# Optimization experiments

Hardware: AMD Instinct MI355X
Metric: run time of the kernel (lower is better)

Reference implementation:

```python
import jax, jax.numpy as jnp
import numpy as np

B, T, D = 2, 2048, 2048
N, KH, H = 16, 8, 128  # query heads, kv heads, head_dim
S = 2048               # cache size
EPS = 1e-6
ROPE_THETA = 1000000.0
K_MASK = -0.7 * float(np.finfo(np.float32).max)  # jax _get_large_negative(float32)


def _rms_norm(x, w):
    rms = jnp.sqrt(jnp.mean(x.astype(jnp.float32) ** 2, axis=-1, keepdims=True) + EPS)
    return (w * x / rms).astype(x.dtype)


def _rope_embeddings(positions, head_dim):
    fraction = jnp.arange(0, head_dim, 2, dtype=jnp.float32) / head_dim
    inv_freq = 1.0 / (ROPE_THETA ** fraction)
    sinusoid = jnp.einsum('BT,k->BTk', positions.astype(jnp.float32), inv_freq,
                          precision=jax.lax.Precision.HIGHEST)
    return jnp.sin(sinusoid), jnp.cos(sinusoid)


def _apply_rope(x, sin, cos):
    h = x.shape[-1] // 2
    x1, x2 = x[..., :h], x[..., h:]
    s, c = sin[:, :, None, :], cos[:, :, None, :]
    return jnp.concatenate([x1 * c - x2 * s, x2 * c + x1 * s], axis=-1).astype(x.dtype)


def _positions_from_segment_ids(seg):
    t = seg.shape[1]
    pos = jnp.arange(t, dtype=jnp.int32)[None, :] - jnp.argmax(seg, axis=1)[:, None]
    return jnp.where(seg != 0, pos, 2 ** 30)


def _num_left_pad(seg):
    return jnp.sum(jnp.cumsum(seg != 0, axis=-1) == 0, axis=-1).astype(jnp.int32)


def _attention(x, q_w, k_w, v_w, o_w, q_norm_w, k_norm_w, k_cache, v_cache,
               segment_ids, start_ind, cur_ind):
    b, t, _ = x.shape
    s = k_cache.shape[1]
    n, kh, h = q_w.shape[1], k_w.shape[1], q_w.shape[2]

    q = _rms_norm(jnp.einsum('BTD,DNH->BTNH', x, q_w), q_norm_w)  # [B,T,N,H]
    k = _rms_norm(jnp.einsum('BSD,DKH->BSKH', x, k_w), k_norm_w)  # [B,T,K,H]
    v = jnp.einsum('BSD,DKH->BSKH', x, v_w)                       # [B,T,K,H]

    start = jnp.where(start_ind < 0, _num_left_pad(segment_ids), start_ind)
    pos = _positions_from_segment_ids(segment_ids) + cur_ind
    sin, cos = _rope_embeddings(pos, h)
    q = _apply_rope(q, sin, cos)
    k = _apply_rope(k, sin, cos)

    # KV-cache update at cur_ind
    k_cache = jax.lax.dynamic_update_slice(k_cache, k, (0, cur_ind, 0, 0))
    v_cache = jax.lax.dynamic_update_slice(v_cache, v, (0, cur_ind, 0, 0))

    # GQA: group query heads per kv head
    qg = q.reshape(b, t, kh, n // kh, h)
    logits = jnp.einsum('BTHGD,BSHD->BHGTS', qg, k_cache) * (h ** -0.5)

    q_pos = cur_ind + jnp.arange(t, dtype=jnp.int32)[None, :] - start[:, None]  # [B,T]
    ts = jnp.arange(s, dtype=jnp.int32)
    kv_seg = (ts[None, :] >= start[:, None]) & (ts[None, :] < cur_ind + t)      # [B,S] bool
    k_pos = ts[None, :] - start[:, None]                                        # [B,S]
    causal = k_pos[:, None, :] <= q_pos[:, :, None]                             # [B,T,S]
    # faithful to original: bool kv segment ids compared against int segment_ids
    seg_mask = kv_seg[:, None, :].astype(segment_ids.dtype) == segment_ids[:, :, None]
    final_mask = (causal & seg_mask)[:, None, None, :, :]                       # [B,1,1,T,S]

    logits = jnp.where(final_mask, logits, K_MASK)
    attn = jax.nn.softmax(logits.astype(jnp.float32), axis=-1).astype(logits.dtype)
    o = jnp.einsum('BHGTS,BSHD->BTHGD', attn, v_cache).reshape(b, t, n, h)
    return jnp.einsum('BTNH,NHD->BTD', o, o_w)


def setup_inputs() -> dict:
    key = jax.random.key(0)
    ks = jax.random.split(key, 5)
    scale = 0.02
    return {
        'x': jax.random.normal(ks[0], (B, T, D), jnp.float32),
        'q_w': jax.random.normal(ks[1], (D, N, H), jnp.float32) * scale,
        'k_w': jax.random.normal(ks[2], (D, KH, H), jnp.float32) * scale,
        'v_w': jax.random.normal(ks[3], (D, KH, H), jnp.float32) * scale,
        'o_w': jax.random.normal(ks[4], (N, H, D), jnp.float32) * scale,
        'q_norm_w': jnp.ones((H,), jnp.float32),
        'k_norm_w': jnp.ones((H,), jnp.float32),
        'k_cache': jnp.zeros((B, S, KH, H), jnp.float32),
        'v_cache': jnp.zeros((B, S, KH, H), jnp.float32),
        'segment_ids': jnp.ones((B, T), jnp.int32),
        'start_ind': jnp.zeros((B,), jnp.int32),
        'cur_ind': 0,
        'right_pads': 0,
    }


def reference(x, q_w, k_w, v_w, o_w, q_norm_w, k_norm_w, k_cache, v_cache,
              segment_ids, start_ind, cur_ind, right_pads):
    # right_pads only advances the cache write pointer (stateful side effect); it
    # does not affect the attention output.
    return _attention(x, q_w, k_w, v_w, o_w, q_norm_w, k_norm_w,
                      k_cache, v_cache, segment_ids, start_ind, cur_ind)
```

## Files before the change

kernel.cpp:

```cpp
#include <hip/hip_runtime.h>
#include <hip/hip_fp16.h>
#include <climits>
#include <math.h>

#define Bc   2
#define Tc   2048
#define Dc   2048
#define Nc   16
#define KHc  8
#define Hc   128
#define Sc   2048

constexpr float EPSc   = 1e-6f;
constexpr float SCALE2 = 0.1275174477984469f;

typedef short short8 __attribute__((ext_vector_type(8)));
typedef _Float16 half8 __attribute__((ext_vector_type(8)));
typedef __fp16 fp16x2 __attribute__((ext_vector_type(2)));
typedef float float4v __attribute__((ext_vector_type(4)));

union U16x8 { uint4 u; short8 s8; half8 h8; unsigned short us[8]; };
union H2U  { fp16x2 h; unsigned u; };
union S8H8 { short8 s; half8 h; };

__device__ __forceinline__ unsigned short f2bf(float f) {
    union { float f; unsigned u; } v; v.f = f;
    unsigned r = v.u + 0x7FFFu + ((v.u >> 16) & 1u);
    return (unsigned short)(r >> 16);
}
__device__ __forceinline__ float bf2f(unsigned short u) {
    union { unsigned u; float f; } v; v.u = ((unsigned)u) << 16;
    return v.f;
}

__device__ __forceinline__ void tc_body(const float* __restrict__ in,
                                        unsigned short* __restrict__ out,
                                        int R, int C, int bx, int by, int tid,
                                        float tile[32][33])
{
    int c0 = bx * 32, r0 = by * 32;
#pragma unroll
    for (int i = 0; i < 4; ++i) {
        int row = (tid >> 5) + i * 8, col = tid & 31;
        tile[row][col] = in[(size_t)(r0 + row) * C + c0 + col];
    }
    __syncthreads();
#pragma unroll
    for (int i = 0; i < 4; ++i) {
        int rowo = (tid >> 5) + i * 8, colo = tid & 31;
        out[(size_t)(c0 + rowo) * R + r0 + colo] = f2bf(tile[colo][rowo]);
    }
}

__global__ __launch_bounds__(256) void prep(const float* __restrict__ x,
                                            const float* __restrict__ qw,
                                            const float* __restrict__ kw,
                                            const float* __restrict__ vw,
                                            const float* __restrict__ ow,
                                            const int* __restrict__ seg,
                                            const int* __restrict__ start_ind,
                                            int* __restrict__ meta,
                                            unsigned short* __restrict__ xb,
                                            unsigned short* __restrict__ qkvwT,
                                            unsigned short* __restrict__ owT)
{
    __shared__ float tile[32][33];
    __shared__ int s_max, s_amax, s_nz;
    int id = blockIdx.x;
    int tid = threadIdx.x;

    if (id < Bc) {
        int b = id;
        if (tid == 0) { s_max = INT_MIN; s_amax = Tc; s_nz = Tc; }
        __syncthreads();
        int lmax = INT_MIN;
        for (int t = tid; t < Tc; t += 256) lmax = max(lmax, seg[b * Tc + t]);
        atomicMax(&s_max, lmax);
        __syncthreads();
        int mv = s_max;
        int lamax = Tc, lnz = Tc;
        for (int t = tid; t < Tc; t += 256) {
            int v = seg[b * Tc + t];
            if (v == mv) lamax = min(lamax, t);
            if (v != 0)  lnz   = min(lnz, t);
        }
        atomicMin(&s_amax, lamax);
        atomicMin(&s_nz, lnz);
        __syncthreads();
        if (tid == 0) {
            meta[b] = s_amax;
            int st = start_ind[b];
            meta[Bc + b] = (st < 0) ? s_nz : st;
        }
        return;
    }
    id -= Bc;
    if (id < 4096) {
        size_t base = ((size_t)id * 256 + tid) * 8;
        float4 a = *(const float4*)&x[base];
        float4 b = *(const float4*)&x[base + 4];
        U16x8 o;
        o.us[0] = f2bf(a.x); o.us[1] = f2bf(a.y); o.us[2] = f2bf(a.z); o.us[3] = f2bf(a.w);
        o.us[4] = f2bf(b.x); o.us[5] = f2bf(b.y); o.us[6] = f2bf(b.z); o.us[7] = f2bf(b.w);
        *(uint4*)&xb[base] = o.u;
        return;
    }
    id -= 4096;
    if (id < 4096) { tc_body(qw, qkvwT, 2048, 2048, id & 63, id >> 6, tid, tile); return; }
    id -= 4096;
    if (id < 2048) { tc_body(kw, qkvwT + (size_t)2048 * 2048, 2048, 1024, id & 31, id >> 5, tid, tile); return; }
    id -= 2048;
    if (id < 2048) { tc_body(vw, qkvwT + (size_t)3072 * 2048, 2048, 1024, id & 31, id >> 5, tid, tile); return; }
    id -= 2048;
    tc_body(ow, owT, 2048, 2048, id & 63, id >> 6, tid, tile);
}

__global__ __launch_bounds__(256, 2) void gemm_mfma(const unsigned short* __restrict__ A,
                                                    const unsigned short* __restrict__ BT,
                                                    void* __restrict__ Cout,
                                                    int M, int N, int K, int out_fp32)
{
    __shared__ __align__(16) unsigned short As[128 * 32];
    __shared__ __align__(16) unsigned short Bs[128 * 32];
    int tid = threadIdx.x;
    int lane = tid & 63, w = tid >> 6;
    int quad = lane >> 4, l15 = lane & 15;
    int bm = blockIdx.y * 128, bn = blockIdx.x * 128;
    int wm = (w >> 1) * 64, wn = (w & 1) * 64;

    int srow = lane >> 2;
    int pl   = lane & 3;
    int sw   = (quad ^ ((l15 >> 1) & 3)) * 8;

    float4v acc[16];
#pragma unroll
    for (int i = 0; i < 16; ++i) acc[i] = (float4v)0.f;

    for (int k0 = 0; k0 < K; k0 += 32) {
        __syncthreads();
#pragma unroll
        for (int c = 0; c < 2; ++c) {
            int j = w * 2 + c;
            int row = j * 16 + srow;
            int pg = pl ^ ((row >> 1) & 3);
            __builtin_amdgcn_global_load_lds(
                (__attribute__((address_space(1))) void*)(A + (size_t)(bm + row) * K + k0 + pg * 8),
                (__attribute__((address_space(3))) void*)(As + j * 512), 16, 0, 0);
            __builtin_amdgcn_global_load_lds(
                (__attribute__((address_space(1))) void*)(BT + (size_t)(bn + row) * K + k0 + pg * 8),
                (__attribute__((address_space(3))) void*)(Bs + j * 512), 16, 0, 0);
        }
        __syncthreads();
        short8 af[4];
#pragma unroll
        for (int mi = 0; mi < 4; ++mi)
            af[mi] = *(const short8*)&As[(wm + mi * 16 + l15) * 32 + sw];
#pragma unroll
        for (int ni = 0; ni < 4; ++ni) {
            short8 bf = *(const short8*)&Bs[(wn + ni * 16 + l15) * 32 + sw];
#pragma unroll
            for (int mi = 0; mi < 4; ++mi)
                acc[mi * 4 + ni] = __builtin_amdgcn_mfma_f32_16x16x32_bf16(af[mi], bf, acc[mi * 4 + ni], 0, 0, 0);
        }
    }

#pragma unroll
    for (int mi = 0; mi < 4; ++mi)
#pragma unroll
        for (int ni = 0; ni < 4; ++ni)
#pragma unroll
            for (int reg = 0; reg < 4; ++reg) {
                int row = bm + wm + mi * 16 + quad * 4 + reg;
                int col = bn + wn + ni * 16 + l15;
                float v = acc[mi * 4 + ni][reg];
                if (out_fp32) ((float*)Cout)[(size_t)row * N + col] = v;
                else ((unsigned short*)Cout)[(size_t)row * N + col] = f2bf(v);
            }
}

__global__ __launch_bounds__(256) void post(unsigned short* __restrict__ QKVh,
                                            unsigned short* __restrict__ Kall,
                                            unsigned short* __restrict__ Vt,
                                            const float* __restrict__ qw,
                                            const float* __restrict__ kw,
                                            const int* __restrict__ seg,
                                            const int* __restrict__ meta,
                                            const int* __restrict__ cur_ptr,
                                            const float* __restrict__ kc,
                                            const float* __restrict__ vc)
{
    int id = blockIdx.x;
    int tid = threadIdx.x;
    int cur = cur_ptr[0];

    if (id < 24576) {
        int rowid = id * 4 + (tid >> 6);
        int lane = tid & 63;
        int hh = rowid % 24;
        int bt = rowid / 24;
        int t = bt & (Tc - 1);
        int b = bt >> 11;

        const unsigned short* in;
        unsigned short* out;
        const float* wt;
        if (hh < 16) {
            unsigned short* p = QKVh + (size_t)bt * 4096 + hh * Hc;
            in = p; out = p; wt = qw;
        } else {
            int kh = hh - 16;
            in = QKVh + (size_t)bt * 4096 + 2048 + kh * Hc;
            out = Kall + (((size_t)b * Sc + cur + t) * KHc + kh) * Hc;
            wt = kw;
        }
        float v1 = bf2f(in[lane]), v2 = bf2f(in[lane + 64]);
        float ssq = v1 * v1 + v2 * v2;
#pragma unroll
        for (int off = 1; off < 64; off <<= 1) ssq += __shfl_xor(ssq, off);
        float rinv = rsqrtf(ssq * (1.0f / Hc) + EPSc);

        int sg = seg[bt];
        long long pos = (sg != 0) ? (long long)(t - meta[b]) : (long long)(1 << 30);
        float posf = (float)(pos + (long long)cur);
        float inv_freq = exp2f(-(float)lane * (19.931568569324174f / 64.0f));
        float s, c;
        sincosf(posf * inv_freq, &s, &c);

        float n1 = wt[lane] * v1 * rinv;
        float n2 = wt[lane + 64] * v2 * rinv;
        out[lane]      = f2bf(n1 * c - n2 * s);
        out[lane + 64] = f2bf(n2 * c + n1 * s);
        return;
    }
    id -= 24576;
    if (id < 2048) {
        size_t base = ((size_t)id * 256 + tid) * 8;
        int s = (int)((base >> 10) & (Sc - 1));
        if (s >= cur && s < cur + Tc) return;
        float4 a = *(const float4*)&kc[base];
        float4 b = *(const float4*)&kc[base + 4];
        U16x8 o;
        o.us[0] = f2bf(a.x); o.us[1] = f2bf(a.y); o.us[2] = f2bf(a.z); o.us[3] = f2bf(a.w);
        o.us[4] = f2bf(b.x); o.us[5] = f2bf(b.y); o.us[6] = f2bf(b.z); o.us[7] = f2bf(b.w);
        *(uint4*)&Kall[base] = o.u;
        return;
    }
    id -= 2048;
    {
        int gid = id * 256 + tid;
        int h  = gid & 127;
        int s8 = ((gid >> 7) & 255) * 8;
        int kh = (gid >> 15) & 7;
        int b  = gid >> 18;
        int curT = cur + Tc;
        unsigned short tmp[8];
#pragma unroll
        for (int e = 0; e < 8; ++e) {
            int s = s8 + e;
            float f;
            if (s >= cur && s < curT)
                f = bf2f(QKVh[(size_t)(b * Tc + (s - cur)) * 4096 + 3072 + kh * Hc + h]);
            else
                f = vc[((size_t)(b * Sc + s) * KHc + kh) * Hc + h];
            tmp[e] = __half_as_ushort(__float2half(f));
        }
        *(uint4*)&Vt[(((size_t)b * KHc + kh) * Hc + h) * Sc + s8] = *(uint4*)tmp;
    }
}

__global__ __launch_bounds__(256, 2) void flash_mfma(const unsigned short* __restrict__ Qb,
                                                     const unsigned short* __restrict__ Kall,
                                                     const unsigned short* __restrict__ Vt,
                                                     const int* __restrict__ seg,
                                                     const int* __restrict__ meta,
                                                     const int* __restrict__ cur_ptr,
                                                     unsigned short* __restrict__ Ob)
{
    __shared__ __align__(16) unsigned short Ks[64 * 128];
    __shared__ __align__(16) unsigned short Vs[128 * 64];
    __shared__ __align__(16) unsigned short Ps[128 * 72];

    int tid = threadIdx.x;
    int lane = tid & 63, w = tid >> 6;
    int quad = lane >> 4, l15 = lane & 15;
    int bid = blockIdx.x;
    int raw = bid & 15;
    int n  = (bid >> 4) & 15;
    int b  = bid >> 8;
    int qt = (b == 0) ? raw : (15 - raw);
    int kh = n >> 1;
    int cur = cur_ptr[0];
    int startb = meta[Bc + b];
    int curT = cur + Tc;
    int t0 = qt * 128 + w * 32;

    short8 qf[2][4];
#pragma unroll
    for (int qtile = 0; qtile < 2; ++qtile)
#pragma unroll
        for (int ks = 0; ks < 4; ++ks) {
            int row = t0 + qtile * 16 + l15;
            U16x8 u;
            u.u = *(const uint4*)&Qb[(size_t)(b * Tc + row) * 4096 + n * Hc + ks * 32 + quad * 8];
            qf[qtile][ks] = u.s8;
        }

    int ctq[2], clsq[2];
#pragma unroll
    for (int qtile = 0; qtile < 2; ++qtile) {
        int trow = t0 + qtile * 16 + l15;
        int sg = seg[b * Tc + trow];
        clsq[qtile] = (sg == 0) ? 0 : ((sg == 1) ? 1 : 2);
        ctq[qtile] = cur + trow;
    }
    unsigned long long m0 = __ballot(clsq[0] == 1);
    unsigned long long m1 = __ballot(clsq[1] == 1);
    bool allseg1 = ((m0 & m1) == 0xFFFFFFFFFFFFFFFFull);

    float lsum[2] = {0.f, 0.f};
    float4v oT[16];
#pragma unroll
    for (int i = 0; i < 16; ++i) oT[i] = (float4v)0.f;

    int s_end = min(Sc, cur + qt * 128 + 128);
    int nch = (s_end + 63) >> 6;

    const size_t kstride = (size_t)KHc * Hc;
    const unsigned short* kptr[4];
    unsigned short* kdst[4];
#pragma unroll
    for (int i = 0; i < 4; ++i) {
        int j = w * 4 + i;
        int row = j * 4 + (lane >> 4);
        int pl = lane & 15;
        int pg = pl ^ ((row >> 1) & 7);
        kptr[i] = Kall + (size_t)b * Sc * kstride + (size_t)row * kstride + kh * Hc + pg * 8;
        kdst[i] = Ks + j * 512;
    }
    const unsigned short* vptr[4];
    unsigned short* vdst[4];
#pragma unroll
    for (int i = 0; i < 4; ++i) {
        int j = w * 4 + i;
        int h = j * 8 + (lane >> 3);
        int pl = lane & 7;
        int pg = pl ^ ((h >> 1) & 7);
        vptr[i] = Vt + ((size_t)b * KHc + kh) * (size_t)Hc * Sc + (size_t)h * Sc + pg * 8;
        vdst[i] = Vs + j * 512;
    }
    int sw3 = (l15 >> 1) & 7;
    unsigned short* psrow0 = Ps + (w * 32 + l15) * 72;
    unsigned short* psrow1 = Ps + (w * 32 + 16 + l15) * 72;

    for (int c = 0; c < nch; ++c) {
        int s0 = c * 64;
#pragma unroll
        for (int i = 0; i < 4; ++i) {
            __builtin_amdgcn_global_load_lds(
                (__attribute__((address_space(1))) void*)(kptr[i] + (size_t)s0 * kstride),
                (__attribute__((address_space(3))) void*)kdst[i], 16, 0, 0);
            __builtin_amdgcn_global_load_lds(
                (__attribute__((address_space(1))) void*)(vptr[i] + s0),
                (__attribute__((address_space(3))) void*)vdst[i], 16, 0, 0);
        }
        __syncthreads();

        float4v st[4][2];
#pragma unroll
        for (int i = 0; i < 4; ++i) { st[i][0] = (float4v)0.f; st[i][1] = (float4v)0.f; }
#pragma unroll
        for (int ks = 0; ks < 4; ++ks) {
#pragma unroll
            for (int stile = 0; stile < 4; ++stile) {
                short8 kf = *(const short8*)&Ks[(stile * 16 + l15) * 128 + ((ks * 4 + quad) ^ sw3) * 8];
                st[stile][0] = __builtin_amdgcn_mfma_f32_16x16x32_bf16(kf, qf[0][ks], st[stile][0], 0, 0, 0);
                st[stile][1] = __builtin_amdgcn_mfma_f32_16x16x32_bf16(kf, qf[1][ks], st[stile][1], 0, 0, 0);
            }
        }

        bool fullok = allseg1 && (s0 >= startb) && (s0 + 63 <= cur + t0) && (s0 + 63 < curT);

#pragma unroll
        for (int stile = 0; stile < 4; ++stile) {
#pragma unroll
            for (int qtile = 0; qtile < 2; ++qtile) {
                float p0, p1, p2, p3;
                if (fullok) {
                    p0 = exp2f(st[stile][qtile][0] * SCALE2);
                    p1 = exp2f(st[stile][qtile][1] * SCALE2);
                    p2 = exp2f(st[stile][qtile][2] * SCALE2);
                    p3 = exp2f(st[stile][qtile][3] * SCALE2);
                } else {
                    int ctv = ctq[qtile], clsv = clsq[qtile];
                    float pp[4];
#pragma unroll
                    for (int reg = 0; reg < 4; ++reg) {
                        int s = s0 + stile * 16 + quad * 4 + reg;
                        int kvseg = (s >= startb && s < curT) ? 1 : 0;
                        bool ok = (s <= ctv) && (clsv == kvseg);
                        pp[reg] = exp2f(ok ? st[stile][qtile][reg] * SCALE2 : -1e30f);
                    }
                    p0 = pp[0]; p1 = pp[1]; p2 = pp[2]; p3 = pp[3];
                }
                lsum[qtile] += (p0 + p1) + (p2 + p3);
                H2U a, d;
                a.h = __builtin_amdgcn_cvt_pkrtz(p0, p1);
                d.h = __builtin_amdgcn_cvt_pkrtz(p2, p3);
                uint2 pk; pk.x = a.u; pk.y = d.u;
                unsigned short* pr = (qtile == 0) ? psrow0 : psrow1;
                *(uint2*)&pr[stile * 16 + quad * 4] = pk;
            }
        }

#pragma unroll
        for (int kk = 0; kk < 2; ++kk) {
            S8H8 pf0, pf1;
            pf0.s = *(const short8*)&psrow0[kk * 32 + quad * 8];
            pf1.s = *(const short8*)&psrow1[kk * 32 + quad * 8];
#pragma unroll
            for (int htile = 0; htile < 8; ++htile) {
                S8H8 vf;
                vf.s = *(const short8*)&Vs[(htile * 16 + l15) * 64 + ((kk * 4 + quad) ^ sw3) * 8];
                oT[htile * 2 + 0] = __builtin_amdgcn_mfma_f32_16x16x32_f16(vf.h, pf0.h, oT[htile * 2 + 0], 0, 0, 0);
                oT[htile * 2 + 1] = __builtin_amdgcn_mfma_f32_16x16x32_f16(vf.h, pf1.h, oT[htile * 2 + 1], 0, 0, 0);
            }
        }
        __syncthreads();
    }

    float linv[2];
#pragma unroll
    for (int qtile = 0; qtile < 2; ++qtile) {
        float l = lsum[qtile];
        l += __shfl_xor(l, 16);
        l += __shfl_xor(l, 32);
        linv[qtile] = (l > 0.f) ? (1.0f / l) : 0.f;
    }

#pragma unroll
    for (int qtile = 0; qtile < 2; ++qtile) {
        int trow = t0 + qtile * 16 + l15;
        size_t base = ((size_t)(b * Tc + trow) * Nc + n) * Hc;
#pragma unroll
        for (int htile = 0; htile < 8; ++htile) {
            float4v v = oT[htile * 2 + qtile];
            unsigned short r0 = f2bf(v[0] * linv[qtile]);
            unsigned short r1 = f2bf(v[1] * linv[qtile]);
            unsigned short r2 = f2bf(v[2] * linv[qtile]);
            unsigned short r3 = f2bf(v[3] * linv[qtile]);
            uint2 pk;
            pk.x = (unsigned)r0 | ((unsigned)r1 << 16);
            pk.y = (unsigned)r2 | ((unsigned)r3 << 16);
            *(uint2*)&Ob[base + htile * 16 + quad * 4] = pk;
        }
    }
}

extern "C" void kernel_launch(void* const* d_in, const int* in_sizes, int n_in,
                              void* d_out, int out_size, void* d_ws, size_t ws_size,
                              hipStream_t stream)
{
    const float* x        = (const float*)d_in[0];
    const float* q_w      = (const float*)d_in[1];
    const float* k_w      = (const float*)d_in[2];
    const float* v_w      = (const float*)d_in[3];
    const float* o_w      = (const float*)d_in[4];
    const float* q_norm_w = (const float*)d_in[5];
    const float* k_norm_w = (const float*)d_in[6];
    const float* k_cache  = (const float*)d_in[7];
    const float* v_cache  = (const float*)d_in[8];
    const int*   seg      = (const int*)d_in[9];
    const int*   startind = (const int*)d_in[10];
    const int*   cur_ptr  = (const int*)d_in[11];
    (void)in_sizes; (void)n_in; (void)out_size; (void)ws_size;

    char* base = (char*)d_ws;
    int* meta = (int*)base;
    unsigned short* QKVh = (unsigned short*)(base + 1024);
    unsigned short* Kall = (unsigned short*)(base + 33555456);
    unsigned short* Vt   = (unsigned short*)(base + 41944064);
    unsigned short* xb   = (unsigned short*)(base + 50332672);
    unsigned short* qkvwT= (unsigned short*)(base + 67109888);
    unsigned short* owT  = (unsigned short*)(base + 83887104);
    unsigned short* Ob   = xb;

    prep<<<Bc + 4096 + 4096 + 2048 + 2048 + 4096, 256, 0, stream>>>(
        x, q_w, k_w, v_w, o_w, seg, startind, meta, xb, qkvwT, owT);

    gemm_mfma<<<dim3(32, 32), 256, 0, stream>>>(xb, qkvwT, QKVh, Bc * Tc, 4096, Dc, 0);

    post<<<24576 + 2048 + 2048, 256, 0, stream>>>(QKVh, Kall, Vt,
        q_norm_w, k_norm_w, seg, meta, cur_ptr, k_cache, v_cache);

    flash_mfma<<<Bc * Nc * (Tc / 128), 256, 0, stream>>>(QKVh, Kall, Vt, seg, meta, cur_ptr, Ob);

    gemm_mfma<<<dim3(16, 32), 256, 0, stream>>>(Ob, owT, d_out, Bc * Tc, Dc, Nc * Hc, 1);
}
```

Baseline: 396.2 us.

## Double-buffer K/V tiles in flash kernel with async prefetch and swizzled P

```diff
diff --git a/kernel.cpp b/kernel.cpp
--- a/kernel.cpp
+++ b/kernel.cpp
@@ -276,9 +276,9 @@
                                                      const int* __restrict__ cur_ptr,
                                                      unsigned short* __restrict__ Ob)
 {
-    __shared__ __align__(16) unsigned short Ks[64 * 128];
-    __shared__ __align__(16) unsigned short Vs[128 * 64];
-    __shared__ __align__(16) unsigned short Ps[128 * 72];
+    __shared__ __align__(16) unsigned short Ks[2][64 * 128];
+    __shared__ __align__(16) unsigned short Vs[2][128 * 64];
+    __shared__ __align__(16) unsigned short Ps[128 * 64];
 
     int tid = threadIdx.x;
     int lane = tid & 63, w = tid >> 6;
@@ -327,7 +327,6 @@
 
     const size_t kstride = (size_t)KHc * Hc;
     const unsigned short* kptr[4];
-    unsigned short* kdst[4];
 #pragma unroll
     for (int i = 0; i < 4; ++i) {
         int j = w * 4 + i;
@@ -335,10 +334,8 @@
         int pl = lane & 15;
         int pg = pl ^ ((row >> 1) & 7);
         kptr[i] = Kall + (size_t)b * Sc * kstride + (size_t)row * kstride + kh * Hc + pg * 8;
-        kdst[i] = Ks + j * 512;
     }
     const unsigned short* vptr[4];
-    unsigned short* vdst[4];
 #pragma unroll
     for (int i = 0; i < 4; ++i) {
         int j = w * 4 + i;
@@ -346,37 +343,62 @@
         int pl = lane & 7;
         int pg = pl ^ ((h >> 1) & 7);
         vptr[i] = Vt + ((size_t)b * KHc + kh) * (size_t)Hc * Sc + (size_t)h * Sc + pg * 8;
-        vdst[i] = Vs + j * 512;
-    }
+    }
+    const int jbase = w * 4 * 512;
     int sw3 = (l15 >> 1) & 7;
-    unsigned short* psrow0 = Ps + (w * 32 + l15) * 72;
-    unsigned short* psrow1 = Ps + (w * 32 + 16 + l15) * 72;
+    int sw8 = l15 & 7;
+    unsigned short* psrow0 = Ps + (w * 32 + l15) * 64;
+    unsigned short* psrow1 = Ps + (w * 32 + 16 + l15) * 64;
+
+#pragma unroll
+    for (int i = 0; i < 4; ++i) {
+        __builtin_amdgcn_global_load_lds(
+            (__attribute__((address_space(1))) void*)(kptr[i]),
+            (__attribute__((address_space(3))) void*)(&Ks[0][jbase + i * 512]), 16, 0, 0);
+        __builtin_amdgcn_global_load_lds(
+            (__attribute__((address_space(1))) void*)(vptr[i]),
+            (__attribute__((address_space(3))) void*)(&Vs[0][jbase + i * 512]), 16, 0, 0);
+    }
 
     for (int c = 0; c < nch; ++c) {
+        const int pb = c & 1;
+        const unsigned short* ksb = &Ks[pb][0];
+        const unsigned short* vsb = &Vs[pb][0];
         int s0 = c * 64;
-#pragma unroll
-        for (int i = 0; i < 4; ++i) {
-            __builtin_amdgcn_global_load_lds(
-                (__attribute__((address_space(1))) void*)(kptr[i] + (size_t)s0 * kstride),
-                (__attribute__((address_space(3))) void*)kdst[i], 16, 0, 0);
-            __builtin_amdgcn_global_load_lds(
-                (__attribute__((address_space(1))) void*)(vptr[i] + s0),
-                (__attribute__((address_space(3))) void*)vdst[i], 16, 0, 0);
-        }
-        __syncthreads();
+
+        if (c + 1 < nch) {
+            const int nb = pb ^ 1;
+            const int s1 = s0 + 64;
+#pragma unroll
+            for (int i = 0; i < 4; ++i) {
+                __builtin_amdgcn_global_load_lds(
+                    (__attribute__((address_space(1))) void*)(kptr[i] + (size_t)s1 * kstride),
+                    (__attribute__((address_space(3))) void*)(&Ks[nb][jbase + i * 512]), 16, 0, 0);
+                __builtin_amdgcn_global_load_lds(
+                    (__attribute__((address_space(1))) void*)(vptr[i] + s1),
+                    (__attribute__((address_space(3))) void*)(&Vs[nb][jbase + i * 512]), 16, 0, 0);
+            }
+            asm volatile("s_waitcnt vmcnt(8)" ::: "memory");
+        } else {
+            asm volatile("s_waitcnt vmcnt(0)" ::: "memory");
+        }
+        __builtin_amdgcn_s_barrier();
+        asm volatile("" ::: "memory");
 
         float4v st[4][2];
 #pragma unroll
         for (int i = 0; i < 4; ++i) { st[i][0] = (float4v)0.f; st[i][1] = (float4v)0.f; }
+        __builtin_amdgcn_s_setprio(1);
 #pragma unroll
         for (int ks = 0; ks < 4; ++ks) {
 #pragma unroll
             for (int stile = 0; stile < 4; ++stile) {
-                short8 kf = *(const short8*)&Ks[(stile * 16 + l15) * 128 + ((ks * 4 + quad) ^ sw3) * 8];
+                short8 kf = *(const short8*)&ksb[(stile * 16 + l15) * 128 + ((ks * 4 + quad) ^ sw3) * 8];
                 st[stile][0] = __builtin_amdgcn_mfma_f32_16x16x32_bf16(kf, qf[0][ks], st[stile][0], 0, 0, 0);
                 st[stile][1] = __builtin_amdgcn_mfma_f32_16x16x32_bf16(kf, qf[1][ks], st[stile][1], 0, 0, 0);
             }
         }
+        __builtin_amdgcn_s_setprio(0);
 
         bool fullok = allseg1 && (s0 >= startb) && (s0 + 63 <= cur + t0) && (s0 + 63 < curT);
 
@@ -408,24 +430,28 @@
                 d.h = __builtin_amdgcn_cvt_pkrtz(p2, p3);
                 uint2 pk; pk.x = a.u; pk.y = d.u;
                 unsigned short* pr = (qtile == 0) ? psrow0 : psrow1;
-                *(uint2*)&pr[stile * 16 + quad * 4] = pk;
+                *(uint2*)&pr[(((stile * 2 + (quad >> 1)) ^ sw8) << 3) + (quad & 1) * 4] = pk;
             }
         }
 
+        __builtin_amdgcn_s_setprio(1);
 #pragma unroll
         for (int kk = 0; kk < 2; ++kk) {
             S8H8 pf0, pf1;
-            pf0.s = *(const short8*)&psrow0[kk * 32 + quad * 8];
-            pf1.s = *(const short8*)&psrow1[kk * 32 + quad * 8];
+            pf0.s = *(const short8*)&psrow0[((kk * 4 + quad) ^ sw8) << 3];
+            pf1.s = *(const short8*)&psrow1[((kk * 4 + quad) ^ sw8) << 3];
 #pragma unroll
             for (int htile = 0; htile < 8; ++htile) {
                 S8H8 vf;
-                vf.s = *(const short8*)&Vs[(htile * 16 + l15) * 64 + ((kk * 4 + quad) ^ sw3) * 8];
+                vf.s = *(const short8*)&vsb[(htile * 16 + l15) * 64 + ((kk * 4 + quad) ^ sw3) * 8];
                 oT[htile * 2 + 0] = __builtin_amdgcn_mfma_f32_16x16x32_f16(vf.h, pf0.h, oT[htile * 2 + 0], 0, 0, 0);
                 oT[htile * 2 + 1] = __builtin_amdgcn_mfma_f32_16x16x32_f16(vf.h, pf1.h, oT[htile * 2 + 1], 0, 0, 0);
             }
         }
-        __syncthreads();
+        __builtin_amdgcn_s_setprio(0);
+
+        asm volatile("" ::: "memory");
+        __builtin_amdgcn_s_barrier();
     }
 
     float linv[2];
```

New measurement: 397.2 us. About the same (+0.2%).

## Shrink flash attention blocks to 64 query rows with reordered grid and swizzled P

Applied to the files above, without the earlier changes.

```diff
diff --git a/kernel.cpp b/kernel.cpp
--- a/kernel.cpp
+++ b/kernel.cpp
@@ -268,31 +268,38 @@
     }
 }
 
-__global__ __launch_bounds__(256, 2) void flash_mfma(const unsigned short* __restrict__ Qb,
-                                                     const unsigned short* __restrict__ Kall,
-                                                     const unsigned short* __restrict__ Vt,
-                                                     const int* __restrict__ seg,
-                                                     const int* __restrict__ meta,
-                                                     const int* __restrict__ cur_ptr,
-                                                     unsigned short* __restrict__ Ob)
+__global__ __launch_bounds__(128) void flash_mfma(const unsigned short* __restrict__ Qb,
+                                                  const unsigned short* __restrict__ Kall,
+                                                  const unsigned short* __restrict__ Vt,
+                                                  const int* __restrict__ seg,
+                                                  const int* __restrict__ meta,
+                                                  const int* __restrict__ cur_ptr,
+                                                  unsigned short* __restrict__ Ob)
 {
     __shared__ __align__(16) unsigned short Ks[64 * 128];
     __shared__ __align__(16) unsigned short Vs[128 * 64];
-    __shared__ __align__(16) unsigned short Ps[128 * 72];
+    __shared__ __align__(16) unsigned short Ps[64 * 64];
 
     int tid = threadIdx.x;
     int lane = tid & 63, w = tid >> 6;
     int quad = lane >> 4, l15 = lane & 15;
     int bid = blockIdx.x;
-    int raw = bid & 15;
-    int n  = (bid >> 4) & 15;
-    int b  = bid >> 8;
-    int qt = (b == 0) ? raw : (15 - raw);
+
+    int k4 = bid >> 8;
+    int u  = (bid >> 5) & 7;
+    int bn = bid & 31;
+    int qt;
+    if      (k4 == 0) qt = u;
+    else if (k4 == 1) qt = 15 - u;
+    else if (k4 == 2) qt = 16 + u;
+    else              qt = 31 - u;
+    int b = bn >> 4;
+    int n = bn & 15;
     int kh = n >> 1;
     int cur = cur_ptr[0];
     int startb = meta[Bc + b];
     int curT = cur + Tc;
-    int t0 = qt * 128 + w * 32;
+    int t0 = qt * 64 + w * 32;
 
     short8 qf[2][4];
 #pragma unroll
@@ -300,9 +307,9 @@
 #pragma unroll
         for (int ks = 0; ks < 4; ++ks) {
             int row = t0 + qtile * 16 + l15;
-            U16x8 u;
-            u.u = *(const uint4*)&Qb[(size_t)(b * Tc + row) * 4096 + n * Hc + ks * 32 + quad * 8];
-            qf[qtile][ks] = u.s8;
+            U16x8 uq;
+            uq.u = *(const uint4*)&Qb[(size_t)(b * Tc + row) * 4096 + n * Hc + ks * 32 + quad * 8];
+            qf[qtile][ks] = uq.s8;
         }
 
     int ctq[2], clsq[2];
@@ -322,26 +329,26 @@
 #pragma unroll
     for (int i = 0; i < 16; ++i) oT[i] = (float4v)0.f;
 
-    int s_end = min(Sc, cur + qt * 128 + 128);
+    int s_end = min(Sc, cur + qt * 64 + 64);
     int nch = (s_end + 63) >> 6;
 
     const size_t kstride = (size_t)KHc * Hc;
-    const unsigned short* kptr[4];
-    unsigned short* kdst[4];
-#pragma unroll
-    for (int i = 0; i < 4; ++i) {
-        int j = w * 4 + i;
+    const unsigned short* kptr[8];
+    unsigned short* kdst[8];
+#pragma unroll
+    for (int i = 0; i < 8; ++i) {
+        int j = w * 8 + i;
         int row = j * 4 + (lane >> 4);
         int pl = lane & 15;
         int pg = pl ^ ((row >> 1) & 7);
         kptr[i] = Kall + (size_t)b * Sc * kstride + (size_t)row * kstride + kh * Hc + pg * 8;
         kdst[i] = Ks + j * 512;
     }
-    const unsigned short* vptr[4];
-    unsigned short* vdst[4];
-#pragma unroll
-    for (int i = 0; i < 4; ++i) {
-        int j = w * 4 + i;
+    const unsigned short* vptr[8];
+    unsigned short* vdst[8];
+#pragma unroll
+    for (int i = 0; i < 8; ++i) {
+        int j = w * 8 + i;
         int h = j * 8 + (lane >> 3);
         int pl = lane & 7;
         int pg = pl ^ ((h >> 1) & 7);
@@ -349,13 +356,14 @@
         vdst[i] = Vs + j * 512;
     }
     int sw3 = (l15 >> 1) & 7;
-    unsigned short* psrow0 = Ps + (w * 32 + l15) * 72;
-    unsigned short* psrow1 = Ps + (w * 32 + 16 + l15) * 72;
+    int sw8 = l15 & 7;
+    unsigned short* psrow0 = Ps + (w * 32 + l15) * 64;
+    unsigned short* psrow1 = Ps + (w * 32 + 16 + l15) * 64;
 
     for (int c = 0; c < nch; ++c) {
         int s0 = c * 64;
 #pragma unroll
-        for (int i = 0; i < 4; ++i) {
+        for (int i = 0; i < 8; ++i) {
             __builtin_amdgcn_global_load_lds(
                 (__attribute__((address_space(1))) void*)(kptr[i] + (size_t)s0 * kstride),
                 (__attribute__((address_space(3))) void*)kdst[i], 16, 0, 0);
@@ -368,6 +376,7 @@
         float4v st[4][2];
 #pragma unroll
         for (int i = 0; i < 4; ++i) { st[i][0] = (float4v)0.f; st[i][1] = (float4v)0.f; }
+        __builtin_amdgcn_s_setprio(1);
 #pragma unroll
         for (int ks = 0; ks < 4; ++ks) {
 #pragma unroll
@@ -377,6 +386,7 @@
                 st[stile][1] = __builtin_amdgcn_mfma_f32_16x16x32_bf16(kf, qf[1][ks], st[stile][1], 0, 0, 0);
             }
         }
+        __builtin_amdgcn_s_setprio(0);
 
         bool fullok = allseg1 && (s0 >= startb) && (s0 + 63 <= cur + t0) && (s0 + 63 < curT);
 
@@ -408,15 +418,16 @@
                 d.h = __builtin_amdgcn_cvt_pkrtz(p2, p3);
                 uint2 pk; pk.x = a.u; pk.y = d.u;
                 unsigned short* pr = (qtile == 0) ? psrow0 : psrow1;
-                *(uint2*)&pr[stile * 16 + quad * 4] = pk;
+                *(uint2*)&pr[(((stile * 2 + (quad >> 1)) ^ sw8) << 3) + (quad & 1) * 4] = pk;
             }
         }
 
+        __builtin_amdgcn_s_setprio(1);
 #pragma unroll
         for (int kk = 0; kk < 2; ++kk) {
             S8H8 pf0, pf1;
-            pf0.s = *(const short8*)&psrow0[kk * 32 + quad * 8];
-            pf1.s = *(const short8*)&psrow1[kk * 32 + quad * 8];
+            pf0.s = *(const short8*)&psrow0[((kk * 4 + quad) ^ sw8) << 3];
+            pf1.s = *(const short8*)&psrow1[((kk * 4 + quad) ^ sw8) << 3];
 #pragma unroll
             for (int htile = 0; htile < 8; ++htile) {
                 S8H8 vf;
@@ -425,6 +436,8 @@
                 oT[htile * 2 + 1] = __builtin_amdgcn_mfma_f32_16x16x32_f16(vf.h, pf1.h, oT[htile * 2 + 1], 0, 0, 0);
             }
         }
+        __builtin_amdgcn_s_setprio(0);
+
         __syncthreads();
     }
 
@@ -492,7 +505,7 @@
     post<<<24576 + 2048 + 2048, 256, 0, stream>>>(QKVh, Kall, Vt,
         q_norm_w, k_norm_w, seg, meta, cur_ptr, k_cache, v_cache);
 
-    flash_mfma<<<Bc * Nc * (Tc / 128), 256, 0, stream>>>(QKVh, Kall, Vt, seg, meta, cur_ptr, Ob);
+    flash_mfma<<<Bc * Nc * (Tc / 64), 128, 0, stream>>>(QKVh, Kall, Vt, seg, meta, cur_ptr, Ob);
 
     gemm_mfma<<<dim3(16, 32), 256, 0, stream>>>(Ob, owT, d_out, Bc * Tc, Dc, Nc * Hc, 1);
 }
```

Measured after the change: 416.7 us. +5.2%, slower.

## Split flash attention work across 8 waves with 16 query rows each

Applied to the files above, without the earlier changes.

```diff
diff --git a/kernel.cpp b/kernel.cpp
--- a/kernel.cpp
+++ b/kernel.cpp
@@ -268,7 +268,7 @@
     }
 }
 
-__global__ __launch_bounds__(256, 2) void flash_mfma(const unsigned short* __restrict__ Qb,
+__global__ __launch_bounds__(512, 4) void flash_mfma(const unsigned short* __restrict__ Qb,
                                                      const unsigned short* __restrict__ Kall,
                                                      const unsigned short* __restrict__ Vt,
                                                      const int* __restrict__ seg,
@@ -278,7 +278,7 @@
 {
     __shared__ __align__(16) unsigned short Ks[64 * 128];
     __shared__ __align__(16) unsigned short Vs[128 * 64];
-    __shared__ __align__(16) unsigned short Ps[128 * 72];
+    __shared__ __align__(16) unsigned short Ps[128 * 64];
 
     int tid = threadIdx.x;
     int lane = tid & 63, w = tid >> 6;
@@ -292,56 +292,49 @@
     int cur = cur_ptr[0];
     int startb = meta[Bc + b];
     int curT = cur + Tc;
-    int t0 = qt * 128 + w * 32;
-
-    short8 qf[2][4];
-#pragma unroll
-    for (int qtile = 0; qtile < 2; ++qtile)
-#pragma unroll
-        for (int ks = 0; ks < 4; ++ks) {
-            int row = t0 + qtile * 16 + l15;
-            U16x8 u;
-            u.u = *(const uint4*)&Qb[(size_t)(b * Tc + row) * 4096 + n * Hc + ks * 32 + quad * 8];
-            qf[qtile][ks] = u.s8;
-        }
-
-    int ctq[2], clsq[2];
-#pragma unroll
-    for (int qtile = 0; qtile < 2; ++qtile) {
-        int trow = t0 + qtile * 16 + l15;
-        int sg = seg[b * Tc + trow];
-        clsq[qtile] = (sg == 0) ? 0 : ((sg == 1) ? 1 : 2);
-        ctq[qtile] = cur + trow;
-    }
-    unsigned long long m0 = __ballot(clsq[0] == 1);
-    unsigned long long m1 = __ballot(clsq[1] == 1);
-    bool allseg1 = ((m0 & m1) == 0xFFFFFFFFFFFFFFFFull);
-
-    float lsum[2] = {0.f, 0.f};
-    float4v oT[16];
-#pragma unroll
-    for (int i = 0; i < 16; ++i) oT[i] = (float4v)0.f;
+    int t0 = qt * 128 + w * 16;
+
+    short8 qf[4];
+#pragma unroll
+    for (int ks = 0; ks < 4; ++ks) {
+        int row = t0 + l15;
+        U16x8 uq;
+        uq.u = *(const uint4*)&Qb[(size_t)(b * Tc + row) * 4096 + n * Hc + ks * 32 + quad * 8];
+        qf[ks] = uq.s8;
+    }
+
+    int trow0 = t0 + l15;
+    int sg0 = seg[b * Tc + trow0];
+    int cls = (sg0 == 0) ? 0 : ((sg0 == 1) ? 1 : 2);
+    int ct  = cur + trow0;
+    unsigned long long mball = __ballot(cls == 1);
+    bool allseg1 = (mball == 0xFFFFFFFFFFFFFFFFull);
+
+    float lsum = 0.f;
+    float4v oT[8];
+#pragma unroll
+    for (int i = 0; i < 8; ++i) oT[i] = (float4v)0.f;
 
     int s_end = min(Sc, cur + qt * 128 + 128);
     int nch = (s_end + 63) >> 6;
 
     const size_t kstride = (size_t)KHc * Hc;
-    const unsigned short* kptr[4];
-    unsigned short* kdst[4];
-#pragma unroll
-    for (int i = 0; i < 4; ++i) {
-        int j = w * 4 + i;
+    const unsigned short* kptr[2];
+    unsigned short* kdst[2];
+#pragma unroll
+    for (int i = 0; i < 2; ++i) {
+        int j = w * 2 + i;
         int row = j * 4 + (lane >> 4);
         int pl = lane & 15;
         int pg = pl ^ ((row >> 1) & 7);
         kptr[i] = Kall + (size_t)b * Sc * kstride + (size_t)row * kstride + kh * Hc + pg * 8;
         kdst[i] = Ks + j * 512;
     }
-    const unsigned short* vptr[4];
-    unsigned short* vdst[4];
-#pragma unroll
-    for (int i = 0; i < 4; ++i) {
-        int j = w * 4 + i;
+    const unsigned short* vptr[2];
+    unsigned short* vdst[2];
+#pragma unroll
+    for (int i = 0; i < 2; ++i) {
+        int j = w * 2 + i;
         int h = j * 8 + (lane >> 3);
         int pl = lane & 7;
         int pg = pl ^ ((h >> 1) & 7);
@@ -349,13 +342,13 @@
         vdst[i] = Vs + j * 512;
     }
     int sw3 = (l15 >> 1) & 7;
-    unsigned short* psrow0 = Ps + (w * 32 + l15) * 72;
-    unsigned short* psrow1 = Ps + (w * 32 + 16 + l15) * 72;
+    int sw8 = l15 & 7;
+    unsigned short* psrow = Ps + (w * 16 + l15) * 64;
 
     for (int c = 0; c < nch; ++c) {
         int s0 = c * 64;
 #pragma unroll
-        for (int i = 0; i < 4; ++i) {
+        for (int i = 0; i < 2; ++i) {
             __builtin_amdgcn_global_load_lds(
                 (__attribute__((address_space(1))) void*)(kptr[i] + (size_t)s0 * kstride),
                 (__attribute__((address_space(3))) void*)kdst[i], 16, 0, 0);
@@ -365,89 +358,81 @@
         }
         __syncthreads();
 
-        float4v st[4][2];
-#pragma unroll
-        for (int i = 0; i < 4; ++i) { st[i][0] = (float4v)0.f; st[i][1] = (float4v)0.f; }
+        float4v st[4];
+#pragma unroll
+        for (int i = 0; i < 4; ++i) st[i] = (float4v)0.f;
+        __builtin_amdgcn_s_setprio(1);
 #pragma unroll
         for (int ks = 0; ks < 4; ++ks) {
 #pragma unroll
             for (int stile = 0; stile < 4; ++stile) {
                 short8 kf = *(const short8*)&Ks[(stile * 16 + l15) * 128 + ((ks * 4 + quad) ^ sw3) * 8];
-                st[stile][0] = __builtin_amdgcn_mfma_f32_16x16x32_bf16(kf, qf[0][ks], st[stile][0], 0, 0, 0);
-                st[stile][1] = __builtin_amdgcn_mfma_f32_16x16x32_bf16(kf, qf[1][ks], st[stile][1], 0, 0, 0);
+                st[stile] = __builtin_amdgcn_mfma_f32_16x16x32_bf16(kf, qf[ks], st[stile], 0, 0, 0);
             }
         }
+        __builtin_amdgcn_s_setprio(0);
 
         bool fullok = allseg1 && (s0 >= startb) && (s0 + 63 <= cur + t0) && (s0 + 63 < curT);
 
 #pragma unroll
         for (int stile = 0; stile < 4; ++stile) {
-#pragma unroll
-            for (int qtile = 0; qtile < 2; ++qtile) {
-                float p0, p1, p2, p3;
-                if (fullok) {
-                    p0 = exp2f(st[stile][qtile][0] * SCALE2);
-                    p1 = exp2f(st[stile][qtile][1] * SCALE2);
-                    p2 = exp2f(st[stile][qtile][2] * SCALE2);
-                    p3 = exp2f(st[stile][qtile][3] * SCALE2);
-                } else {
-                    int ctv = ctq[qtile], clsv = clsq[qtile];
-                    float pp[4];
-#pragma unroll
-                    for (int reg = 0; reg < 4; ++reg) {
-                        int s = s0 + stile * 16 + quad * 4 + reg;
-                        int kvseg = (s >= startb && s < curT) ? 1 : 0;
-                        bool ok = (s <= ctv) && (clsv == kvseg);
-                        pp[reg] = exp2f(ok ? st[stile][qtile][reg] * SCALE2 : -1e30f);
-                    }
-                    p0 = pp[0]; p1 = pp[1]; p2 = pp[2]; p3 = pp[3];
+            float p0, p1, p2, p3;
+            if (fullok) {
+                p0 = exp2f(st[stile][0] * SCALE2);
+                p1 = exp2f(st[stile][1] * SCALE2);
+                p2 = exp2f(st[stile][2] * SCALE2);
+                p3 = exp2f(st[stile][3] * SCALE2);
+            } else {
+                float pp[4];
+#pragma unroll
+                for (int reg = 0; reg < 4; ++reg) {
+                    int s = s0 + stile * 16 + quad * 4 + reg;
+                    int kvseg = (s >= startb && s < curT) ? 1 : 0;
+                    bool ok = (s <= ct) && (cls == kvseg);
+                    pp[reg] = exp2f(ok ? st[stile][reg] * SCALE2 : -1e30f);
                 }
-                lsum[qtile] += (p0 + p1) + (p2 + p3);
-                H2U a, d;
-                a.h = __builtin_amdgcn_cvt_pkrtz(p0, p1);
-                d.h = __builtin_amdgcn_cvt_pkrtz(p2, p3);
-                uint2 pk; pk.x = a.u; pk.y = d.u;
-                unsigned short* pr = (qtile == 0) ? psrow0 : psrow1;
-                *(uint2*)&pr[stile * 16 + quad * 4] = pk;
+                p0 = pp[0]; p1 = pp[1]; p2 = pp[2]; p3 = pp[3];
             }
-        }
-
+            lsum += (p0 + p1) + (p2 + p3);
+            H2U a, d;
+            a.h = __builtin_amdgcn_cvt_pkrtz(p0, p1);
+            d.h = __builtin_amdgcn_cvt_pkrtz(p2, p3);
+            uint2 pk; pk.x = a.u; pk.y = d.u;
+            *(uint2*)&psrow[(((stile * 2 + (quad >> 1)) ^ sw8) << 3) + (quad & 1) * 4] = pk;
+        }
+
+        __builtin_amdgcn_s_setprio(1);
 #pragma unroll
         for (int kk = 0; kk < 2; ++kk) {
-            S8H8 pf0, pf1;
-            pf0.s = *(const short8*)&psrow0[kk * 32 + quad * 8];
-            pf1.s = *(const short8*)&psrow1[kk * 32 + quad * 8];
+            S8H8 pf;
+            pf.s = *(const short8*)&psrow[((kk * 4 + quad) ^ sw8) << 3];
 #pragma unroll
             for (int htile = 0; htile < 8; ++htile) {
                 S8H8 vf;
                 vf.s = *(const short8*)&Vs[(htile * 16 + l15) * 64 + ((kk * 4 + quad) ^ sw3) * 8];
-                oT[htile * 2 + 0] = __builtin_amdgcn_mfma_f32_16x16x32_f16(vf.h, pf0.h, oT[htile * 2 + 0], 0, 0, 0);
-                oT[htile * 2 + 1] = __builtin_amdgcn_mfma_f32_16x16x32_f16(vf.h, pf1.h, oT[htile * 2 + 1], 0, 0, 0);
+                oT[htile] = __builtin_amdgcn_mfma_f32_16x16x32_f16(vf.h, pf.h, oT[htile], 0, 0, 0);
             }
         }
-        __syncthreads();
-    }
-
-    float linv[2];
-#pragma unroll
-    for (int qtile = 0; qtile < 2; ++qtile) {
-        float l = lsum[qtile];
-        l += __shfl_xor(l, 16);
-        l += __shfl_xor(l, 32);
-        linv[qtile] = (l > 0.f) ? (1.0f / l) : 0.f;
-    }
-
-#pragma unroll
-    for (int qtile = 0; qtile < 2; ++qtile) {
-        int trow = t0 + qtile * 16 + l15;
+        __builtin_amdgcn_s_setprio(0);
+
+        __syncthreads();
+    }
+
+    float l = lsum;
+    l += __shfl_xor(l, 16);
+    l += __shfl_xor(l, 32);
+    float linv = (l > 0.f) ? (1.0f / l) : 0.f;
+
+    {
+        int trow = t0 + l15;
         size_t base = ((size_t)(b * Tc + trow) * Nc + n) * Hc;
 #pragma unroll
         for (int htile = 0; htile < 8; ++htile) {
-            float4v v = oT[htile * 2 + qtile];
-            unsigned short r0 = f2bf(v[0] * linv[qtile]);
-            unsigned short r1 = f2bf(v[1] * linv[qtile]);
-            unsigned short r2 = f2bf(v[2] * linv[qtile]);
-            unsigned short r3 = f2bf(v[3] * linv[qtile]);
+            float4v v = oT[htile];
+            unsigned short r0 = f2bf(v[0] * linv);
+            unsigned short r1 = f2bf(v[1] * linv);
+            unsigned short r2 = f2bf(v[2] * linv);
+            unsigned short r3 = f2bf(v[3] * linv);
             uint2 pk;
             pk.x = (unsigned)r0 | ((unsigned)r1 << 16);
             pk.y = (unsigned)r2 | ((unsigned)r3 << 16);
@@ -492,7 +477,7 @@
     post<<<24576 + 2048 + 2048, 256, 0, stream>>>(QKVh, Kall, Vt,
         q_norm_w, k_norm_w, seg, meta, cur_ptr, k_cache, v_cache);
 
-    flash_mfma<<<Bc * Nc * (Tc / 128), 256, 0, stream>>>(QKVh, Kall, Vt, seg, meta, cur_ptr, Ob);
+    flash_mfma<<<Bc * Nc * (Tc / 128), 512, 0, stream>>>(QKVh, Kall, Vt, seg, meta, cur_ptr, Ob);
 
     gemm_mfma<<<dim3(16, 32), 256, 0, stream>>>(Ob, owT, d_out, Bc * Tc, Dc, Nc * Hc, 1);
 }
```

Measured after the change: 379.1 us. 4.3% less time.
